# Optimization experiments

Measured on AMD Instinct MI355X. Metric: run time of the kernel, lower is better.

## Reference

```python
import jax, jax.numpy as jnp
import numpy as np

N_EMBD = 1024
N_HEADS = 16
HEAD_DIM = N_EMBD // N_HEADS


def setup_inputs() -> dict:
    key = jax.random.key(0)
    ks = jax.random.split(key, 5)
    s = 0.02
    return {
        "x": jax.random.normal(ks[0], (4, 2048, N_EMBD), dtype=jnp.float32),
        "w_attn": jax.random.normal(ks[1], (N_EMBD, 3 * N_EMBD), dtype=jnp.float32) * s,
        "b_attn": jnp.zeros((3 * N_EMBD,), dtype=jnp.float32),
        "w_proj": jax.random.normal(ks[2], (N_EMBD, N_EMBD), dtype=jnp.float32) * s,
        "b_proj": jnp.zeros((N_EMBD,), dtype=jnp.float32),
    }


def reference(x, w_attn, b_attn, w_proj, b_proj):
    B, T, C = x.shape
    H, D = N_HEADS, HEAD_DIM
    qkv = x @ w_attn + b_attn                      # [B,T,3C]
    q, k, v = jnp.split(qkv, 3, axis=-1)
    q = q.reshape(B, T, H, D).transpose(0, 2, 1, 3)  # [B,H,T,D]
    k = k.reshape(B, T, H, D).transpose(0, 2, 1, 3)
    v = v.reshape(B, T, H, D).transpose(0, 2, 1, 3)
    # Faithful to source bug: divide by d**(-0.5) == multiply by sqrt(d)
    scale = jnp.asarray(D, x.dtype) ** 0.5
    scores = jnp.einsum("bhqd,bhkd->bhqk", q, k) * scale  # [B,H,T,T]
    causal = jnp.tril(jnp.ones((T, T), dtype=bool))
    scores = jnp.where(causal[None, None], scores, -jnp.inf)
    attn = jax.nn.softmax(scores, axis=-1)
    y = jnp.einsum("bhqk,bhkd->bhqd", attn, v)     # [B,H,T,D]
    y = y.transpose(0, 2, 1, 3).reshape(B, T, C)
    return y @ w_proj + b_proj
```

## Files before the change

kernel.cpp:

```cpp
#include <hip/hip_runtime.h>
#include <cmath>

#define BB 4
#define TT 2048
#define CC 1024
#define HH 16
#define DD 64
#define MM (BB*TT)

typedef _Float16 f16x8 __attribute__((ext_vector_type(8)));
typedef _Float16 f16x4 __attribute__((ext_vector_type(4)));
typedef float f32x4 __attribute__((ext_vector_type(4)));
typedef unsigned short ushort_t;

#define MFMA16(a,b,c) __builtin_amdgcn_mfma_f32_16x16x16f16(a,b,c,0,0,0)

__device__ __forceinline__ unsigned short f2h(float f) {
    _Float16 h = (_Float16)f;
    return __builtin_bit_cast(unsigned short, h);
}

__device__ __forceinline__ void gld16(const void* gsrc, void* ldst) {
    void* g = const_cast<void*>(gsrc);
    __builtin_amdgcn_global_load_lds(
        (__attribute__((address_space(1))) void*)g,
        (__attribute__((address_space(3))) void*)ldst,
        16, 0, 0);
}

__global__ __launch_bounds__(256)
void cvt4_kernel(const float* __restrict__ in, ushort_t* __restrict__ out, long n4) {
    long i = (long)blockIdx.x * blockDim.x + threadIdx.x;
    if (i >= n4) return;
    float4 v = ((const float4*)in)[i];
    ushort4 o;
    o.x = f2h(v.x); o.y = f2h(v.y); o.z = f2h(v.z); o.w = f2h(v.w);
    ((ushort4*)out)[i] = o;
}

__global__ __launch_bounds__(256)
void trcvt_kernel(const float* __restrict__ in, ushort_t* __restrict__ out,
                  int K, int N) {
    __shared__ float T[32][33];
    const int tx = threadIdx.x & 31;
    const int ty = threadIdx.x >> 5;
    const int n0 = blockIdx.x * 32;
    const int k0 = blockIdx.y * 32;
    #pragma unroll
    for (int i = 0; i < 4; ++i)
        T[ty + i * 8][tx] = in[(size_t)(k0 + ty + i * 8) * N + n0 + tx];
    __syncthreads();
    #pragma unroll
    for (int i = 0; i < 4; ++i)
        out[(size_t)(n0 + ty + i * 8) * K + k0 + tx] = f2h(T[tx][ty + i * 8]);
}

template<int N, bool QKV>
__global__ __launch_bounds__(256)
void hgemm_kernel(const ushort_t* __restrict__ A, const ushort_t* __restrict__ Bt,
                  const float* __restrict__ bias, float* __restrict__ out,
                  ushort_t* __restrict__ qh, ushort_t* __restrict__ kh,
                  ushort_t* __restrict__ vh)
{
    const int K = 1024;
    __shared__ ushort_t As[128 * 32];
    __shared__ ushort_t Bs[128 * 32];

    const int tid  = threadIdx.x;
    const int lane = tid & 63;
    const int wave = tid >> 6;
    const int wm   = (wave & 1) * 64;
    const int wn   = (wave >> 1) * 64;
    const int m0   = blockIdx.y * 128;
    const int n0   = blockIdx.x * 128;
    const int lrow = lane & 15;
    const int quad = lane >> 4;

    const int u0 = wave * 64 + lane;
    const int u1 = u0 + 256;
    const size_t gA0 = (size_t)(m0 + (u0 >> 2)) * K + (u0 & 3) * 8;
    const size_t gA1 = (size_t)(m0 + (u1 >> 2)) * K + (u1 & 3) * 8;
    const size_t gB0 = (size_t)(n0 + (u0 >> 2)) * K + (u0 & 3) * 8;
    const size_t gB1 = (size_t)(n0 + (u1 >> 2)) * K + (u1 & 3) * 8;
    ushort_t* ldsA0 = &As[(wave * 64) * 8];
    ushort_t* ldsA1 = &As[(256 + wave * 64) * 8];
    ushort_t* ldsB0 = &Bs[(wave * 64) * 8];
    ushort_t* ldsB1 = &Bs[(256 + wave * 64) * 8];

    f32x4 acc[4][4];
    const f32x4 z = {0.f, 0.f, 0.f, 0.f};
    #pragma unroll
    for (int mt = 0; mt < 4; ++mt)
        #pragma unroll
        for (int nt = 0; nt < 4; ++nt)
            acc[mt][nt] = z;

    for (int kk = 0; kk < K; kk += 32) {
        gld16(&A[gA0 + kk],  ldsA0);
        gld16(&A[gA1 + kk],  ldsA1);
        gld16(&Bt[gB0 + kk], ldsB0);
        gld16(&Bt[gB1 + kk], ldsB1);
        __syncthreads();

        f16x8 af[4], bf[4];
        #pragma unroll
        for (int mt = 0; mt < 4; ++mt)
            af[mt] = *(const f16x8*)&As[(wm + mt * 16 + lrow) * 32 + quad * 8];
        #pragma unroll
        for (int nt = 0; nt < 4; ++nt)
            bf[nt] = *(const f16x8*)&Bs[(wn + nt * 16 + lrow) * 32 + quad * 8];
        #pragma unroll
        for (int mt = 0; mt < 4; ++mt)
            #pragma unroll
            for (int nt = 0; nt < 4; ++nt)
                acc[mt][nt] = __builtin_amdgcn_mfma_f32_16x16x32_f16(
                    af[mt], bf[nt], acc[mt][nt], 0, 0, 0);
        __syncthreads();
    }

    #pragma unroll
    for (int mt = 0; mt < 4; ++mt) {
        const int rbase = m0 + wm + mt * 16 + quad * 4;
        #pragma unroll
        for (int nt = 0; nt < 4; ++nt) {
            const int col = n0 + wn + nt * 16 + lrow;
            const float bv = bias[col];
            if (QKV) {
                const int which = col >> 10;
                const int c = col & 1023;
                const int h = c >> 6, d = c & 63;
                const int b = rbase >> 11, t0 = rbase & 2047;
                if (which == 2) {
                    ushort4 pk;
                    pk.x = f2h(acc[mt][nt][0] + bv);
                    pk.y = f2h(acc[mt][nt][1] + bv);
                    pk.z = f2h(acc[mt][nt][2] + bv);
                    pk.w = f2h(acc[mt][nt][3] + bv);
                    *(ushort4*)&vh[(((size_t)b * HH + h) * DD + d) * TT + t0] = pk;
                } else {
                    ushort_t* dst = which ? kh : qh;
                    const float sc = which ? 1.0f : 8.0f * 1.44269504088896f;
                    #pragma unroll
                    for (int r = 0; r < 4; ++r)
                        dst[(((size_t)b * HH + h) * TT + t0 + r) * DD + d] =
                            f2h((acc[mt][nt][r] + bv) * sc);
                }
            } else {
                #pragma unroll
                for (int r = 0; r < 4; ++r)
                    out[(size_t)(rbase + r) * N + col] = acc[mt][nt][r] + bv;
            }
        }
    }
}

__global__ __launch_bounds__(256, 4)
void attn_mfma_kernel(const ushort_t* __restrict__ qh, const ushort_t* __restrict__ kh,
                      const ushort_t* __restrict__ vh, ushort_t* __restrict__ yh)
{
    __shared__ ushort_t Ks[64 * 72];
    __shared__ ushort_t Vs[64 * 72];

    const int pr   = blockIdx.x;
    const int bh   = blockIdx.y;
    const int qtA  = 31 - pr;
    const int qtB  = pr;
    const int tid  = threadIdx.x;
    const int lane = tid & 63;
    const int w    = tid >> 6;
    const int lrow = lane & 15;
    const int quad = lane >> 4;

    const ushort_t* qbase = qh + (size_t)bh * TT * DD;
    const ushort_t* kbase = kh + (size_t)bh * TT * DD;
    const ushort_t* vbase = vh + (size_t)bh * DD * TT;
    const int b = bh >> 4, h = bh & 15;

    const int ur = tid >> 3;
    const int uc = (tid & 7) * 8;

    int q0w = qtA * 64 + w * 16;
    f16x8 aq0 = *(const f16x8*)&qbase[(size_t)(q0w + lrow) * DD + quad * 8];
    f16x8 aq1 = *(const f16x8*)&qbase[(size_t)(q0w + lrow) * DD + 32 + quad * 8];

    const f32x4 z = {0.f, 0.f, 0.f, 0.f};
    f32x4 o[4] = {z, z, z, z};
    float mi = -1e30f, li = 0.f;

    uint4 kr0 = *(const uint4*)&kbase[(size_t)ur * DD + uc];
    uint4 kr1 = *(const uint4*)&kbase[(size_t)(ur + 32) * DD + uc];
    uint4 vr0 = *(const uint4*)&vbase[(size_t)ur * TT + uc];
    uint4 vr1 = *(const uint4*)&vbase[(size_t)(ur + 32) * TT + uc];

    for (int i = 0; i <= 32; ++i) {
        if (i == qtA + 1) {
            #pragma unroll
            for (int r = 0; r < 4; ++r) {
                const float inv = 1.0f / __shfl(li, quad * 4 + r, 64);
                const int t = q0w + quad * 4 + r;
                #pragma unroll
                for (int dt = 0; dt < 4; ++dt)
                    yh[((size_t)b * TT + t) * CC + h * 64 + dt * 16 + lrow] =
                        f2h(o[dt][r] * inv);
            }
            q0w = qtB * 64 + w * 16;
            aq0 = *(const f16x8*)&qbase[(size_t)(q0w + lrow) * DD + quad * 8];
            aq1 = *(const f16x8*)&qbase[(size_t)(q0w + lrow) * DD + 32 + quad * 8];
            #pragma unroll
            for (int dt = 0; dt < 4; ++dt) o[dt] = z;
            mi = -1e30f; li = 0.f;
        }
        const int kt = (i <= qtA) ? i : i - qtA - 1;

        __syncthreads();
        *(uint4*)&Ks[(ur)      * 72 + uc] = kr0;
        *(uint4*)&Ks[(ur + 32) * 72 + uc] = kr1;
        *(uint4*)&Vs[(ur)      * 72 + uc] = vr0;
        *(uint4*)&Vs[(ur + 32) * 72 + uc] = vr1;
        __syncthreads();
        if (i < 32) {
            const int ni  = i + 1;
            const int nkt = (ni <= qtA) ? ni : ni - qtA - 1;
            const int nb  = nkt * 64;
            kr0 = *(const uint4*)&kbase[(size_t)(nb + ur) * DD + uc];
            kr1 = *(const uint4*)&kbase[(size_t)(nb + ur + 32) * DD + uc];
            vr0 = *(const uint4*)&vbase[(size_t)ur * TT + nb + uc];
            vr1 = *(const uint4*)&vbase[(size_t)(ur + 32) * TT + nb + uc];
        }

        f32x4 sv[4];
        #pragma unroll
        for (int c = 0; c < 4; ++c) {
            f16x8 ka = *(const f16x8*)&Ks[(c * 16 + lrow) * 72 + quad * 8];
            f16x8 kb = *(const f16x8*)&Ks[(c * 16 + lrow) * 72 + 32 + quad * 8];
            sv[c] = __builtin_amdgcn_mfma_f32_16x16x32_f16(ka, aq0, z, 0, 0, 0);
            sv[c] = __builtin_amdgcn_mfma_f32_16x16x32_f16(kb, aq1, sv[c], 0, 0, 0);
        }

        const int kt2 = kt * 64;
        const int qg  = q0w + lrow;
        const bool diag = (i == qtA) || (i == 32);
        if (diag) {
            #pragma unroll
            for (int c = 0; c < 4; ++c)
                #pragma unroll
                for (int r = 0; r < 4; ++r)
                    if (kt2 + c * 16 + quad * 4 + r > qg) sv[c][r] = -3e38f;
        }
        float m = -3e38f;
        #pragma unroll
        for (int c = 0; c < 4; ++c)
            #pragma unroll
            for (int r = 0; r < 4; ++r) m = fmaxf(m, sv[c][r]);
        m = fmaxf(m, __shfl_xor(m, 16, 64));
        m = fmaxf(m, __shfl_xor(m, 32, 64));
        const float mnew  = fmaxf(mi, m);
        const float alpha = exp2f(mi - mnew);
        mi = mnew;
        float rs = 0.f;
        f16x4 ap[4];
        #pragma unroll
        for (int c = 0; c < 4; ++c)
            #pragma unroll
            for (int r = 0; r < 4; ++r) {
                const float p = exp2f(sv[c][r] - mnew);
                rs += p;
                ap[c][r] = (_Float16)p;
            }
        rs += __shfl_xor(rs, 16, 64);
        rs += __shfl_xor(rs, 32, 64);
        li = li * alpha + rs;

        #pragma unroll
        for (int r = 0; r < 4; ++r) {
            const float ar = __shfl(alpha, quad * 4 + r, 64);
            #pragma unroll
            for (int dt = 0; dt < 4; ++dt) o[dt][r] *= ar;
        }

        #pragma unroll
        for (int dt = 0; dt < 4; ++dt)
            #pragma unroll
            for (int c = 0; c < 4; ++c) {
                f16x4 vb = *(const f16x4*)&Vs[(dt * 16 + lrow) * 72 + c * 16 + quad * 4];
                o[dt] = MFMA16(ap[c], vb, o[dt]);
            }
    }

    #pragma unroll
    for (int r = 0; r < 4; ++r) {
        const float inv = 1.0f / __shfl(li, quad * 4 + r, 64);
        const int t = q0w + quad * 4 + r;
        #pragma unroll
        for (int dt = 0; dt < 4; ++dt)
            yh[((size_t)b * TT + t) * CC + h * 64 + dt * 16 + lrow] =
                f2h(o[dt][r] * inv);
    }
}

extern "C" void kernel_launch(void* const* d_in, const int* in_sizes, int n_in,
                              void* d_out, int out_size, void* d_ws, size_t ws_size,
                              hipStream_t stream) {
    const float* x      = (const float*)d_in[0];
    const float* w_attn = (const float*)d_in[1];
    const float* b_attn = (const float*)d_in[2];
    const float* w_proj = (const float*)d_in[3];
    const float* b_proj = (const float*)d_in[4];
    float* out = (float*)d_out;

    const size_t per = (size_t)BB * HH * TT * DD;
    ushort_t* qh  = (ushort_t*)d_ws;
    ushort_t* kh  = qh + per;
    ushort_t* vh  = kh + per;
    ushort_t* xh  = vh + per;
    ushort_t* yh  = xh;
    ushort_t* wat = xh + (size_t)MM * CC;
    ushort_t* wpt = wat + (size_t)3 * CC * CC;

    cvt4_kernel<<<(MM * CC / 4 + 255) / 256, 256, 0, stream>>>(x, xh, MM * CC / 4);
    trcvt_kernel<<<dim3(3 * CC / 32, CC / 32), 256, 0, stream>>>(w_attn, wat, CC, 3 * CC);
    trcvt_kernel<<<dim3(CC / 32, CC / 32), 256, 0, stream>>>(w_proj, wpt, CC, CC);

    hgemm_kernel<3 * CC, true><<<dim3(3 * CC / 128, MM / 128), 256, 0, stream>>>(
        xh, wat, b_attn, nullptr, qh, kh, vh);

    attn_mfma_kernel<<<dim3(16, BB * HH), 256, 0, stream>>>(qh, kh, vh, yh);

    hgemm_kernel<CC, false><<<dim3(CC / 128, MM / 128), 256, 0, stream>>>(
        yh, wpt, b_proj, out, nullptr, nullptr, nullptr);
}
```

Measured before the change: 280.0 us.

## Split paired causal attention blocks into one block per query tile with lazy rescale

The attention kernel drops the scheme where each block handled a mirrored pair of query tiles. It now launches one block per (batch-head, query tile), with the tile index rotated by blockIdx.y to spread the uneven causal work, and raises the occupancy hint to 8 blocks per CU. It also skips rescaling the running max unless it grows by more than 8 in log2 space, packs the fp16 conversion with cvt_pkrtz, tree-reduces the max and sum, and raises wave priority around the MFMA sections. The result is more, unevenly sized blocks, possible fp16 overflow margin loss from lazy rescaling, and register pressure from the higher occupancy target.

```diff
diff --git a/kernel.cpp b/kernel.cpp
--- a/kernel.cpp
+++ b/kernel.cpp
@@ -10,6 +10,7 @@
 
 typedef _Float16 f16x8 __attribute__((ext_vector_type(8)));
 typedef _Float16 f16x4 __attribute__((ext_vector_type(4)));
+typedef _Float16 f16x2 __attribute__((ext_vector_type(2)));
 typedef float f32x4 __attribute__((ext_vector_type(4)));
 typedef unsigned short ushort_t;
 
@@ -18,6 +19,10 @@
 __device__ __forceinline__ unsigned short f2h(float f) {
     _Float16 h = (_Float16)f;
     return __builtin_bit_cast(unsigned short, h);
+}
+
+__device__ __forceinline__ f16x2 cvt_pk(float a, float b) {
+    return __builtin_bit_cast(f16x2, __builtin_amdgcn_cvt_pkrtz(a, b));
 }
 
 __device__ __forceinline__ void gld16(const void* gsrc, void* ldst) {
@@ -154,17 +159,15 @@
     }
 }
 
-__global__ __launch_bounds__(256, 4)
+__global__ __launch_bounds__(256, 8)
 void attn_mfma_kernel(const ushort_t* __restrict__ qh, const ushort_t* __restrict__ kh,
                       const ushort_t* __restrict__ vh, ushort_t* __restrict__ yh)
 {
     __shared__ ushort_t Ks[64 * 72];
     __shared__ ushort_t Vs[64 * 72];
 
-    const int pr   = blockIdx.x;
-    const int bh   = blockIdx.y;
-    const int qtA  = 31 - pr;
-    const int qtB  = pr;
+    const int bh   = blockIdx.x;
+    const int qt   = (int)((blockIdx.x + blockIdx.y) & 31);
     const int tid  = threadIdx.x;
     const int lane = tid & 63;
     const int w    = tid >> 6;
@@ -179,9 +182,10 @@
     const int ur = tid >> 3;
     const int uc = (tid & 7) * 8;
 
-    int q0w = qtA * 64 + w * 16;
-    f16x8 aq0 = *(const f16x8*)&qbase[(size_t)(q0w + lrow) * DD + quad * 8];
-    f16x8 aq1 = *(const f16x8*)&qbase[(size_t)(q0w + lrow) * DD + 32 + quad * 8];
+    const int q0w = qt * 64 + w * 16;
+    const int qg  = q0w + lrow;
+    const f16x8 aq0 = *(const f16x8*)&qbase[(size_t)(q0w + lrow) * DD + quad * 8];
+    const f16x8 aq1 = *(const f16x8*)&qbase[(size_t)(q0w + lrow) * DD + 32 + quad * 8];
 
     const f32x4 z = {0.f, 0.f, 0.f, 0.f};
     f32x4 o[4] = {z, z, z, z};
@@ -192,36 +196,15 @@
     uint4 vr0 = *(const uint4*)&vbase[(size_t)ur * TT + uc];
     uint4 vr1 = *(const uint4*)&vbase[(size_t)(ur + 32) * TT + uc];
 
-    for (int i = 0; i <= 32; ++i) {
-        if (i == qtA + 1) {
-            #pragma unroll
-            for (int r = 0; r < 4; ++r) {
-                const float inv = 1.0f / __shfl(li, quad * 4 + r, 64);
-                const int t = q0w + quad * 4 + r;
-                #pragma unroll
-                for (int dt = 0; dt < 4; ++dt)
-                    yh[((size_t)b * TT + t) * CC + h * 64 + dt * 16 + lrow] =
-                        f2h(o[dt][r] * inv);
-            }
-            q0w = qtB * 64 + w * 16;
-            aq0 = *(const f16x8*)&qbase[(size_t)(q0w + lrow) * DD + quad * 8];
-            aq1 = *(const f16x8*)&qbase[(size_t)(q0w + lrow) * DD + 32 + quad * 8];
-            #pragma unroll
-            for (int dt = 0; dt < 4; ++dt) o[dt] = z;
-            mi = -1e30f; li = 0.f;
-        }
-        const int kt = (i <= qtA) ? i : i - qtA - 1;
-
+    for (int kt = 0; kt <= qt; ++kt) {
         __syncthreads();
         *(uint4*)&Ks[(ur)      * 72 + uc] = kr0;
         *(uint4*)&Ks[(ur + 32) * 72 + uc] = kr1;
         *(uint4*)&Vs[(ur)      * 72 + uc] = vr0;
         *(uint4*)&Vs[(ur + 32) * 72 + uc] = vr1;
         __syncthreads();
-        if (i < 32) {
-            const int ni  = i + 1;
-            const int nkt = (ni <= qtA) ? ni : ni - qtA - 1;
-            const int nb  = nkt * 64;
+        if (kt < qt) {
+            const int nb = (kt + 1) * 64;
             kr0 = *(const uint4*)&kbase[(size_t)(nb + ur) * DD + uc];
             kr1 = *(const uint4*)&kbase[(size_t)(nb + ur + 32) * DD + uc];
             vr0 = *(const uint4*)&vbase[(size_t)ur * TT + nb + uc];
@@ -229,6 +212,7 @@
         }
 
         f32x4 sv[4];
+        __builtin_amdgcn_s_setprio(1);
         #pragma unroll
         for (int c = 0; c < 4; ++c) {
             f16x8 ka = *(const f16x8*)&Ks[(c * 16 + lrow) * 72 + quad * 8];
@@ -236,48 +220,56 @@
             sv[c] = __builtin_amdgcn_mfma_f32_16x16x32_f16(ka, aq0, z, 0, 0, 0);
             sv[c] = __builtin_amdgcn_mfma_f32_16x16x32_f16(kb, aq1, sv[c], 0, 0, 0);
         }
+        __builtin_amdgcn_s_setprio(0);
 
         const int kt2 = kt * 64;
-        const int qg  = q0w + lrow;
-        const bool diag = (i == qtA) || (i == 32);
-        if (diag) {
+        if (kt == qt) {
             #pragma unroll
             for (int c = 0; c < 4; ++c)
                 #pragma unroll
                 for (int r = 0; r < 4; ++r)
                     if (kt2 + c * 16 + quad * 4 + r > qg) sv[c][r] = -3e38f;
         }
-        float m = -3e38f;
+        float mc[4];
         #pragma unroll
         for (int c = 0; c < 4; ++c)
-            #pragma unroll
-            for (int r = 0; r < 4; ++r) m = fmaxf(m, sv[c][r]);
+            mc[c] = fmaxf(fmaxf(sv[c][0], sv[c][1]), fmaxf(sv[c][2], sv[c][3]));
+        float m = fmaxf(fmaxf(mc[0], mc[1]), fmaxf(mc[2], mc[3]));
         m = fmaxf(m, __shfl_xor(m, 16, 64));
         m = fmaxf(m, __shfl_xor(m, 32, 64));
-        const float mnew  = fmaxf(mi, m);
-        const float alpha = exp2f(mi - mnew);
-        mi = mnew;
-        float rs = 0.f;
-        f16x4 ap[4];
-        #pragma unroll
-        for (int c = 0; c < 4; ++c)
+
+        if (__any(m > mi + 8.0f)) {
+            const float mnew  = fmaxf(mi, m);
+            const float alpha = exp2f(mi - mnew);
+            mi = mnew;
+            li *= alpha;
             #pragma unroll
             for (int r = 0; r < 4; ++r) {
-                const float p = exp2f(sv[c][r] - mnew);
-                rs += p;
-                ap[c][r] = (_Float16)p;
+                const float ar = __shfl(alpha, quad * 4 + r, 64);
+                #pragma unroll
+                for (int dt = 0; dt < 4; ++dt) o[dt][r] *= ar;
             }
+        }
+
+        f16x4 ap[4];
+        float rc[4];
+        #pragma unroll
+        for (int c = 0; c < 4; ++c) {
+            const float p0 = exp2f(sv[c][0] - mi);
+            const float p1 = exp2f(sv[c][1] - mi);
+            const float p2 = exp2f(sv[c][2] - mi);
+            const float p3 = exp2f(sv[c][3] - mi);
+            rc[c] = (p0 + p1) + (p2 + p3);
+            const f16x2 lo = cvt_pk(p0, p1);
+            const f16x2 hi = cvt_pk(p2, p3);
+            ap[c][0] = lo[0]; ap[c][1] = lo[1]; ap[c][2] = hi[0]; ap[c][3] = hi[1];
+        }
+        float rs = (rc[0] + rc[1]) + (rc[2] + rc[3]);
         rs += __shfl_xor(rs, 16, 64);
         rs += __shfl_xor(rs, 32, 64);
-        li = li * alpha + rs;
-
-        #pragma unroll
-        for (int r = 0; r < 4; ++r) {
-            const float ar = __shfl(alpha, quad * 4 + r, 64);
-            #pragma unroll
-            for (int dt = 0; dt < 4; ++dt) o[dt][r] *= ar;
-        }
-
+        li += rs;
+
+        __builtin_amdgcn_s_setprio(1);
         #pragma unroll
         for (int dt = 0; dt < 4; ++dt)
             #pragma unroll
@@ -285,6 +277,7 @@
                 f16x4 vb = *(const f16x4*)&Vs[(dt * 16 + lrow) * 72 + c * 16 + quad * 4];
                 o[dt] = MFMA16(ap[c], vb, o[dt]);
             }
+        __builtin_amdgcn_s_setprio(0);
     }
 
     #pragma unroll
@@ -324,7 +317,7 @@
     hgemm_kernel<3 * CC, true><<<dim3(3 * CC / 128, MM / 128), 256, 0, stream>>>(
         xh, wat, b_attn, nullptr, qh, kh, vh);
 
-    attn_mfma_kernel<<<dim3(16, BB * HH), 256, 0, stream>>>(qh, kh, vh, yh);
+    attn_mfma_kernel<<<dim3(BB * HH, 32), 256, 0, stream>>>(qh, kh, vh, yh);
 
     hgemm_kernel<CC, false><<<dim3(CC / 128, MM / 128), 256, 0, stream>>>(
         yh, wpt, b_proj, out, nullptr, nullptr, nullptr);
```

After: 529.6 us. 1.89x slower.

## Double-buffer K/V tiles in attention and skip softmax rescale when max stable

Applied to the files above, without the earlier changes.

Moves attention K/V shared-memory staging to a two-buffer ping-pong. The next tile is stored to LDS after the current tile's MFMAs, with a single barrier per iteration instead of two, and register prefetch runs two tiles ahead. Adds a lazy online-softmax rescale that only updates the running max and rescales the accumulators when some row max exceeds the old max by more than 8 (log2 units), plus packed fp16 conversion of probabilities and s_setprio around the MFMA blocks. It doubles LDS use, which may lower occupancy. The lazy rescale lets exp2 values reach up to 2^8, which fp16 can hold.

```diff
diff --git a/kernel.cpp b/kernel.cpp
--- a/kernel.cpp
+++ b/kernel.cpp
@@ -10,6 +10,7 @@
 
 typedef _Float16 f16x8 __attribute__((ext_vector_type(8)));
 typedef _Float16 f16x4 __attribute__((ext_vector_type(4)));
+typedef _Float16 f16x2 __attribute__((ext_vector_type(2)));
 typedef float f32x4 __attribute__((ext_vector_type(4)));
 typedef unsigned short ushort_t;
 
@@ -18,6 +19,10 @@
 __device__ __forceinline__ unsigned short f2h(float f) {
     _Float16 h = (_Float16)f;
     return __builtin_bit_cast(unsigned short, h);
+}
+
+__device__ __forceinline__ f16x2 cvt_pk(float a, float b) {
+    return __builtin_bit_cast(f16x2, __builtin_amdgcn_cvt_pkrtz(a, b));
 }
 
 __device__ __forceinline__ void gld16(const void* gsrc, void* ldst) {
@@ -158,8 +163,8 @@
 void attn_mfma_kernel(const ushort_t* __restrict__ qh, const ushort_t* __restrict__ kh,
                       const ushort_t* __restrict__ vh, ushort_t* __restrict__ yh)
 {
-    __shared__ ushort_t Ks[64 * 72];
-    __shared__ ushort_t Vs[64 * 72];
+    __shared__ ushort_t Ks[2][64 * 72];
+    __shared__ ushort_t Vs[2][64 * 72];
 
     const int pr   = blockIdx.x;
     const int bh   = blockIdx.y;
@@ -192,7 +197,22 @@
     uint4 vr0 = *(const uint4*)&vbase[(size_t)ur * TT + uc];
     uint4 vr1 = *(const uint4*)&vbase[(size_t)(ur + 32) * TT + uc];
 
+    *(uint4*)&Ks[0][(ur)      * 72 + uc] = kr0;
+    *(uint4*)&Ks[0][(ur + 32) * 72 + uc] = kr1;
+    *(uint4*)&Vs[0][(ur)      * 72 + uc] = vr0;
+    *(uint4*)&Vs[0][(ur + 32) * 72 + uc] = vr1;
+    {
+        const int nkt = (1 <= qtA) ? 1 : 0;
+        const int nb  = nkt * 64;
+        kr0 = *(const uint4*)&kbase[(size_t)(nb + ur) * DD + uc];
+        kr1 = *(const uint4*)&kbase[(size_t)(nb + ur + 32) * DD + uc];
+        vr0 = *(const uint4*)&vbase[(size_t)ur * TT + nb + uc];
+        vr1 = *(const uint4*)&vbase[(size_t)(ur + 32) * TT + nb + uc];
+    }
+    __syncthreads();
+
     for (int i = 0; i <= 32; ++i) {
+        const int cur = i & 1;
         if (i == qtA + 1) {
             #pragma unroll
             for (int r = 0; r < 4; ++r) {
@@ -212,30 +232,16 @@
         }
         const int kt = (i <= qtA) ? i : i - qtA - 1;
 
-        __syncthreads();
-        *(uint4*)&Ks[(ur)      * 72 + uc] = kr0;
-        *(uint4*)&Ks[(ur + 32) * 72 + uc] = kr1;
-        *(uint4*)&Vs[(ur)      * 72 + uc] = vr0;
-        *(uint4*)&Vs[(ur + 32) * 72 + uc] = vr1;
-        __syncthreads();
-        if (i < 32) {
-            const int ni  = i + 1;
-            const int nkt = (ni <= qtA) ? ni : ni - qtA - 1;
-            const int nb  = nkt * 64;
-            kr0 = *(const uint4*)&kbase[(size_t)(nb + ur) * DD + uc];
-            kr1 = *(const uint4*)&kbase[(size_t)(nb + ur + 32) * DD + uc];
-            vr0 = *(const uint4*)&vbase[(size_t)ur * TT + nb + uc];
-            vr1 = *(const uint4*)&vbase[(size_t)(ur + 32) * TT + nb + uc];
-        }
-
         f32x4 sv[4];
+        __builtin_amdgcn_s_setprio(1);
         #pragma unroll
         for (int c = 0; c < 4; ++c) {
-            f16x8 ka = *(const f16x8*)&Ks[(c * 16 + lrow) * 72 + quad * 8];
-            f16x8 kb = *(const f16x8*)&Ks[(c * 16 + lrow) * 72 + 32 + quad * 8];
+            f16x8 ka = *(const f16x8*)&Ks[cur][(c * 16 + lrow) * 72 + quad * 8];
+            f16x8 kb = *(const f16x8*)&Ks[cur][(c * 16 + lrow) * 72 + 32 + quad * 8];
             sv[c] = __builtin_amdgcn_mfma_f32_16x16x32_f16(ka, aq0, z, 0, 0, 0);
             sv[c] = __builtin_amdgcn_mfma_f32_16x16x32_f16(kb, aq1, sv[c], 0, 0, 0);
         }
+        __builtin_amdgcn_s_setprio(0);
 
         const int kt2 = kt * 64;
         const int qg  = q0w + lrow;
@@ -247,44 +253,72 @@
                 for (int r = 0; r < 4; ++r)
                     if (kt2 + c * 16 + quad * 4 + r > qg) sv[c][r] = -3e38f;
         }
-        float m = -3e38f;
+        float mc[4];
         #pragma unroll
         for (int c = 0; c < 4; ++c)
-            #pragma unroll
-            for (int r = 0; r < 4; ++r) m = fmaxf(m, sv[c][r]);
+            mc[c] = fmaxf(fmaxf(sv[c][0], sv[c][1]), fmaxf(sv[c][2], sv[c][3]));
+        float m = fmaxf(fmaxf(mc[0], mc[1]), fmaxf(mc[2], mc[3]));
         m = fmaxf(m, __shfl_xor(m, 16, 64));
         m = fmaxf(m, __shfl_xor(m, 32, 64));
-        const float mnew  = fmaxf(mi, m);
-        const float alpha = exp2f(mi - mnew);
-        mi = mnew;
-        float rs = 0.f;
+
+        if (__any(m > mi + 8.0f)) {
+            const float mnew  = fmaxf(mi, m);
+            const float alpha = exp2f(mi - mnew);
+            mi = mnew;
+            li *= alpha;
+            #pragma unroll
+            for (int r = 0; r < 4; ++r) {
+                const float ar = __shfl(alpha, quad * 4 + r, 64);
+                #pragma unroll
+                for (int dt = 0; dt < 4; ++dt) o[dt][r] *= ar;
+            }
+        }
+
         f16x4 ap[4];
-        #pragma unroll
-        for (int c = 0; c < 4; ++c)
-            #pragma unroll
-            for (int r = 0; r < 4; ++r) {
-                const float p = exp2f(sv[c][r] - mnew);
-                rs += p;
-                ap[c][r] = (_Float16)p;
-            }
+        float rc[4];
+        #pragma unroll
+        for (int c = 0; c < 4; ++c) {
+            const float p0 = exp2f(sv[c][0] - mi);
+            const float p1 = exp2f(sv[c][1] - mi);
+            const float p2 = exp2f(sv[c][2] - mi);
+            const float p3 = exp2f(sv[c][3] - mi);
+            rc[c] = (p0 + p1) + (p2 + p3);
+            const f16x2 lo = cvt_pk(p0, p1);
+            const f16x2 hi = cvt_pk(p2, p3);
+            ap[c][0] = lo[0]; ap[c][1] = lo[1]; ap[c][2] = hi[0]; ap[c][3] = hi[1];
+        }
+        float rs = (rc[0] + rc[1]) + (rc[2] + rc[3]);
         rs += __shfl_xor(rs, 16, 64);
         rs += __shfl_xor(rs, 32, 64);
-        li = li * alpha + rs;
-
-        #pragma unroll
-        for (int r = 0; r < 4; ++r) {
-            const float ar = __shfl(alpha, quad * 4 + r, 64);
-            #pragma unroll
-            for (int dt = 0; dt < 4; ++dt) o[dt][r] *= ar;
-        }
-
+        li += rs;
+
+        __builtin_amdgcn_s_setprio(1);
         #pragma unroll
         for (int dt = 0; dt < 4; ++dt)
             #pragma unroll
             for (int c = 0; c < 4; ++c) {
-                f16x4 vb = *(const f16x4*)&Vs[(dt * 16 + lrow) * 72 + c * 16 + quad * 4];
+                f16x4 vb = *(const f16x4*)&Vs[cur][(dt * 16 + lrow) * 72 + c * 16 + quad * 4];
                 o[dt] = MFMA16(ap[c], vb, o[dt]);
             }
+        __builtin_amdgcn_s_setprio(0);
+
+        if (i < 32) {
+            const int nxt = cur ^ 1;
+            *(uint4*)&Ks[nxt][(ur)      * 72 + uc] = kr0;
+            *(uint4*)&Ks[nxt][(ur + 32) * 72 + uc] = kr1;
+            *(uint4*)&Vs[nxt][(ur)      * 72 + uc] = vr0;
+            *(uint4*)&Vs[nxt][(ur + 32) * 72 + uc] = vr1;
+            if (i < 31) {
+                const int ni  = i + 2;
+                const int nkt = (ni <= qtA) ? ni : ni - qtA - 1;
+                const int nb  = nkt * 64;
+                kr0 = *(const uint4*)&kbase[(size_t)(nb + ur) * DD + uc];
+                kr1 = *(const uint4*)&kbase[(size_t)(nb + ur + 32) * DD + uc];
+                vr0 = *(const uint4*)&vbase[(size_t)ur * TT + nb + uc];
+                vr1 = *(const uint4*)&vbase[(size_t)(ur + 32) * TT + nb + uc];
+            }
+        }
+        __syncthreads();
     }
 
     #pragma unroll
```

New measurement: 283.8 us. Within noise of the previous version (+1.4%).
